# Kernel optimization log

Measured on AMD Instinct MI355X. Metric: run time of the kernel, lower is better.

Reference implementation:

```python
import jax, jax.numpy as jnp
import numpy as np

EMBED_DIM = 1024
HEAD = 16
DK = EMBED_DIM // HEAD  # 64
B, S = 2, 2048
NEG = -1.0e9


def setup_inputs() -> dict:
    key = jax.random.key(0)
    ks = jax.random.split(key, 8)
    d = {
        'query': jax.random.normal(ks[0], (B, S, EMBED_DIM), jnp.float32),
        'key': jax.random.normal(ks[1], (B, S, EMBED_DIM), jnp.float32),
        'value': jax.random.normal(ks[2], (B, S, EMBED_DIM), jnp.float32),
        'masked': jax.random.randint(ks[3], (B, S, S), 0, 2).astype(bool),
        'Wq': jax.random.normal(ks[4], (EMBED_DIM, EMBED_DIM), jnp.float32) / np.sqrt(EMBED_DIM),
        'Wk': jax.random.normal(ks[5], (EMBED_DIM, EMBED_DIM), jnp.float32) / np.sqrt(EMBED_DIM),
        'Wv': jax.random.normal(ks[6], (EMBED_DIM, EMBED_DIM), jnp.float32) / np.sqrt(EMBED_DIM),
        'Wo': jax.random.normal(ks[7], (EMBED_DIM, EMBED_DIM), jnp.float32) / np.sqrt(EMBED_DIM),
    }
    return d


def reference(query, key, value, masked, Wq, Wk, Wv, Wo):
    # projections (bias-free Linear: x @ W), split into heads: [B, H, S, DK]
    def split_heads(x):
        b, s, _ = x.shape
        return x.reshape(b, s, HEAD, DK).transpose(0, 2, 1, 3)

    q = split_heads(query @ Wq)
    k = split_heads(key @ Wk)
    v = split_heads(value @ Wv)

    scale = 1.0 / jnp.sqrt(jnp.asarray(DK, q.dtype))
    scores = jnp.einsum('bhqd,bhkd->bhqk', q, k) * scale
    scores = jnp.where(masked[:, None, :, :], NEG, scores)
    attn = jax.nn.softmax(scores, axis=-1)
    out = jnp.einsum('bhqk,bhkd->bhqd', attn, v)  # [B, H, S, DK]
    out = out.transpose(0, 2, 1, 3).reshape(query.shape[0], -1, EMBED_DIM)
    return out @ Wo
```

## Files before the change

kernel.cpp:

```cpp
#include <hip/hip_runtime.h>
#include <hip/hip_bf16.h>

typedef float f32x4 __attribute__((ext_vector_type(4)));
typedef __bf16 bf16x8 __attribute__((ext_vector_type(8)));

__device__ __forceinline__ unsigned short f2bf(float f){
  unsigned int u = __builtin_bit_cast(unsigned int, f);
  u += 0x7fffu + ((u >> 16) & 1u);
  return (unsigned short)(u >> 16);
}
__device__ __forceinline__ float bf2f(unsigned short h){
  return __builtin_bit_cast(float, (unsigned int)h << 16);
}

__device__ __forceinline__ void glds16(const void* g, void* l){
  __builtin_amdgcn_global_load_lds((const __attribute__((address_space(1))) void*)g,
                                   (__attribute__((address_space(3))) void*)l, 16, 0, 0);
}

__device__ __forceinline__ f32x4 mfma16(bf16x8 a, bf16x8 b, f32x4 c){
  return __builtin_amdgcn_mfma_f32_16x16x32_bf16(a, b, c, 0, 0, 0);
}

#if __has_builtin(__builtin_amdgcn_exp2f)
__device__ __forceinline__ float exp2v(float x){ return __builtin_amdgcn_exp2f(x); }
#else
__device__ __forceinline__ float exp2v(float x){ return exp2f(x); }
#endif

__device__ __forceinline__ unsigned int cvtpk(float a, float b){
  unsigned int r;
  asm("v_cvt_pk_bf16_f32 %0, %1, %2" : "=v"(r) : "v"(a), "v"(b));
  return r;
}

__global__ void detect_kernel(const unsigned int* __restrict__ m, int* __restrict__ flag){
  int t = threadIdx.x;
  int bad = 0;
  for(int i = t; i < 4096; i += 256) bad |= (m[i] > 1u);
  unsigned long long b = __ballot(bad != 0);
  __shared__ int sbuf[4];
  if((t & 63) == 0) sbuf[t >> 6] = (b != 0ull);
  __syncthreads();
  if(t == 0) flag[0] = (sbuf[0] | sbuf[1] | sbuf[2] | sbuf[3]) ? 0 : 1;
}

__global__ void pack_mask_kernel(const unsigned char* __restrict__ m8,
                                 unsigned int* __restrict__ mp,
                                 const int* __restrict__ flag){
  const int wid = threadIdx.x >> 6, lane = threadIdx.x & 63;
  const int row = blockIdx.x * 4 + wid;
  const int is32 = flag[0];
  const int* m32 = (const int*)m8;
  for(int c0 = 0; c0 < 2048; c0 += 64){
    int mv = is32 ? m32[(size_t)row*2048 + c0 + lane]
                  : (int)m8[(size_t)row*2048 + c0 + lane];
    unsigned long long b = __ballot(mv != 0);
    if(lane == 0){
      mp[(size_t)row*64 + (c0 >> 5)]     = (unsigned int)b;
      mp[(size_t)row*64 + (c0 >> 5) + 1] = (unsigned int)(b >> 32);
    }
  }
}

__global__ void cvt_kernel(const float* __restrict__ src, unsigned short* __restrict__ dst){
  int i = blockIdx.x * 256 + threadIdx.x;
  const float4* s = (const float4*)src;
  float4 a = s[2*i], b = s[2*i+1];
  union { unsigned short h[8]; uint4 v; } o;
  o.h[0]=f2bf(a.x); o.h[1]=f2bf(a.y); o.h[2]=f2bf(a.z); o.h[3]=f2bf(a.w);
  o.h[4]=f2bf(b.x); o.h[5]=f2bf(b.y); o.h[6]=f2bf(b.z); o.h[7]=f2bf(b.w);
  ((uint4*)dst)[i] = o.v;
}

__global__ void transW_kernel(const float* __restrict__ Wq, const float* __restrict__ Wk,
                              const float* __restrict__ Wv, const float* __restrict__ Wo,
                              unsigned short* __restrict__ WT){
  const float* W = (blockIdx.y==0)?Wq:(blockIdx.y==1)?Wk:(blockIdx.y==2)?Wv:Wo;
  unsigned short* D = WT + (size_t)blockIdx.y * 1048576;
  int r0 = (blockIdx.x >> 4) * 64, c0 = (blockIdx.x & 15) * 64;
  __shared__ unsigned short T[64][65];
  int t = threadIdx.x;
  {
    int r = t >> 2, cb = (t & 3) * 16;
    const float4* src = (const float4*)(W + (size_t)(r0 + r) * 1024 + (c0 + cb));
    float4 v0 = src[0], v1 = src[1], v2 = src[2], v3 = src[3];
    float vals[16] = {v0.x,v0.y,v0.z,v0.w, v1.x,v1.y,v1.z,v1.w,
                      v2.x,v2.y,v2.z,v2.w, v3.x,v3.y,v3.z,v3.w};
    #pragma unroll
    for(int j=0;j<16;j++) T[cb + j][r] = f2bf(vals[j]);
  }
  __syncthreads();
  {
    int c = t >> 2, rb = (t & 3) * 16;
    union { unsigned short h[16]; uint4 v[2]; } o;
    #pragma unroll
    for(int j=0;j<16;j++) o.h[j] = T[c][rb + j];
    uint4* dp = (uint4*)(D + (size_t)(c0 + c) * 1024 + (r0 + rb));
    dp[0] = o.v[0]; dp[1] = o.v[1];
  }
}

__global__ void transV_kernel(const unsigned short* __restrict__ Vb,
                              unsigned short* __restrict__ Vt){
  const int bh = blockIdx.y, b = bh >> 4, h = bh & 15;
  const int s0 = blockIdx.x * 64;
  __shared__ unsigned short T[64][68];
  const int t = threadIdx.x;
  {
    int r = t >> 2, cb = (t & 3) * 16;
    const uint4* src = (const uint4*)(Vb + (size_t)(b*2048 + s0 + r)*1024 + h*64 + cb);
    union { unsigned short h[16]; uint4 v[2]; } o;
    o.v[0] = src[0]; o.v[1] = src[1];
    uint2* dst = (uint2*)&T[r][cb];
    const uint2* sv = (const uint2*)o.h;
    dst[0]=sv[0]; dst[1]=sv[1]; dst[2]=sv[2]; dst[3]=sv[3];
  }
  __syncthreads();
  {
    int c = t >> 2, sb = (t & 3) * 16;
    union { unsigned short h[16]; uint4 v[2]; } o;
    #pragma unroll
    for(int j=0;j<16;j++) o.h[j] = T[sb + j][c];
    uint4* dp = (uint4*)(Vt + (size_t)(bh*64 + c)*2048 + s0 + sb);
    dp[0] = o.v[0]; dp[1] = o.v[1];
  }
}

template<int OUTF32>
__global__ __launch_bounds__(256,2) void gemm_bt(
    const unsigned short* __restrict__ A0, const unsigned short* __restrict__ A1, const unsigned short* __restrict__ A2,
    const unsigned short* __restrict__ B0, const unsigned short* __restrict__ B1, const unsigned short* __restrict__ B2,
    unsigned short* __restrict__ C0, unsigned short* __restrict__ C1, unsigned short* __restrict__ C2,
    float* __restrict__ Cf)
{
  const unsigned short* A  = (blockIdx.z==0)?A0:(blockIdx.z==1)?A1:A2;
  const unsigned short* BT = (blockIdx.z==0)?B0:(blockIdx.z==1)?B1:B2;
  unsigned short* C        = (blockIdx.z==0)?C0:(blockIdx.z==1)?C1:C2;
  __shared__ unsigned short Asm[128*32];
  __shared__ unsigned short Bsm[128*32];
  const int wid = threadIdx.x >> 6, lane = threadIdx.x & 63;
  const int m0 = blockIdx.x * 128, n0 = blockIdx.y * 128;
  const int wrow = wid >> 1, wcol = wid & 1;
  f32x4 acc[4][4] = {};
  const int sr = lane >> 2;
  const int sc = lane & 3;

  for(int kt = 0; kt < 32; ++kt){
    const int kofs = kt * 32;
    #pragma unroll
    for(int i=0;i<2;i++){
      int r = wid*32 + i*16 + sr;
      int blk = sc ^ (r & 3);
      glds16(A  + (size_t)(m0 + r)*1024 + kofs + blk*8, &Asm[(wid*32 + i*16)*32]);
      glds16(BT + (size_t)(n0 + r)*1024 + kofs + blk*8, &Bsm[(wid*32 + i*16)*32]);
    }
    __syncthreads();
    bf16x8 af[4], bfv[4];
    #pragma unroll
    for(int fm=0; fm<4; fm++){
      int row = wrow*64 + fm*16 + (lane & 15);
      int blk = (lane >> 4) ^ (row & 3);
      af[fm] = *(const bf16x8*)&Asm[row*32 + blk*8];
    }
    #pragma unroll
    for(int fn=0; fn<4; fn++){
      int row = wcol*64 + fn*16 + (lane & 15);
      int blk = (lane >> 4) ^ (row & 3);
      bfv[fn] = *(const bf16x8*)&Bsm[row*32 + blk*8];
    }
    __builtin_amdgcn_s_setprio(1);
    #pragma unroll
    for(int fm=0; fm<4; fm++)
      #pragma unroll
      for(int fn=0; fn<4; fn++)
        acc[fm][fn] = mfma16(af[fm], bfv[fn], acc[fm][fn]);
    __builtin_amdgcn_s_setprio(0);
    __syncthreads();
  }
  #pragma unroll
  for(int fm=0; fm<4; fm++){
    #pragma unroll
    for(int fn=0; fn<4; fn++){
      int col  = n0 + wcol*64 + fn*16 + (lane & 15);
      int rowb = m0 + wrow*64 + fm*16 + (lane >> 4)*4;
      #pragma unroll
      for(int r=0;r<4;r++){
        if(OUTF32) Cf[(size_t)(rowb + r)*1024 + col] = acc[fm][fn][r];
        else       C [(size_t)(rowb + r)*1024 + col] = f2bf(acc[fm][fn][r]);
      }
    }
  }
}

__global__ __launch_bounds__(256,4) void attn_kernel(
    const unsigned short* __restrict__ Q, const unsigned short* __restrict__ K,
    const unsigned short* __restrict__ Vt, unsigned short* __restrict__ O,
    const unsigned int* __restrict__ mp)
{
  __shared__ unsigned short Ksm[2][64*64];
  __shared__ unsigned short Vsm[2][64*64];
  __shared__ unsigned short Psm[4][16][64];
  const int wid = threadIdx.x >> 6, lane = threadIdx.x & 63;
  const int orig = blockIdx.x;
  const int wg = (orig & 7) * 128 + (orig >> 3);
  const int qt = wg & 31, bh = wg >> 5;
  const int b = bh >> 4, h = bh & 15;
  const int q0 = qt * 64;
  const int li = lane & 15, lg = lane >> 4;

  bf16x8 qf[2];
  {
    const unsigned short* qp = Q + (size_t)(b*2048 + q0 + wid*16 + li)*1024 + h*64 + lg*8;
    union { unsigned short s[8]; bf16x8 v; } u0, u1;
    u0.v = *(const bf16x8*)qp; u1.v = *(const bf16x8*)(qp + 32);
    #pragma unroll
    for(int j=0;j<8;j++){
      u0.s[j] = f2bf(bf2f(u0.s[j]) * 0.1803368801111601f);
      u1.s[j] = f2bf(bf2f(u1.s[j]) * 0.1803368801111601f);
    }
    qf[0] = u0.v; qf[1] = u1.v;
  }

  f32x4 oacc[4] = {};
  float mrow = -__builtin_inff();
  float lrow = 0.f;

  const int srow = lane >> 3;
  const int sblk = (lane & 7) ^ srow;
  const int mrowg = b*2048 + q0 + wid*16 + li;
  const int li7 = li & 7;

  #pragma unroll
  for(int i=0;i<2;i++){
    int r = wid*16 + i*8 + srow;
    glds16(K  + (size_t)(b*2048 + r)*1024 + h*64 + sblk*8, &Ksm[0][(wid*16 + i*8)*64]);
    glds16(Vt + (size_t)(bh*64 + r)*2048 + sblk*8,         &Vsm[0][(wid*16 + i*8)*64]);
  }
  uint2 mw = *(const uint2*)&mp[(size_t)mrowg*64];
  uint2 mwn;
  __syncthreads();

  int buf = 0;
  for(int t = 0; t < 32; ++t){
    const int kv0 = t * 64;
    if(t < 31){
      #pragma unroll
      for(int i=0;i<2;i++){
        int r = wid*16 + i*8 + srow;
        glds16(K  + (size_t)(b*2048 + kv0 + 64 + r)*1024 + h*64 + sblk*8, &Ksm[buf^1][(wid*16 + i*8)*64]);
        glds16(Vt + (size_t)(bh*64 + r)*2048 + kv0 + 64 + sblk*8,         &Vsm[buf^1][(wid*16 + i*8)*64]);
      }
      mwn = *(const uint2*)&mp[(size_t)mrowg*64 + (size_t)((kv0 + 64) >> 5)];
    }
    float p[4][4];
    __builtin_amdgcn_s_setprio(1);
    #pragma unroll
    for(int f=0; f<4; f++){
      f32x4 s = {0.f,0.f,0.f,0.f};
      #pragma unroll
      for(int kf=0; kf<2; kf++){
        int blk = (kf*4 + lg) ^ li7;
        bf16x8 kfr = *(const bf16x8*)&Ksm[buf][(f*16 + li)*64 + blk*8];
        s = mfma16(kfr, qf[kf], s);
      }
      #pragma unroll
      for(int j=0;j<4;j++) p[f][j] = s[j];
    }
    __builtin_amdgcn_s_setprio(0);
    #pragma unroll
    for(int f=0; f<4; f++){
      unsigned int w = (f < 2) ? mw.x : mw.y;
      #pragma unroll
      for(int j=0;j<4;j++){
        unsigned int bit = (w >> ((f & 1)*16 + lg*4 + j)) & 1u;
        p[f][j] = bit ? -1.0e9f : p[f][j];
      }
    }
    float tmax;
    {
      float m0 = fmaxf(fmaxf(p[0][0],p[0][1]), fmaxf(p[0][2],p[0][3]));
      float m1 = fmaxf(fmaxf(p[1][0],p[1][1]), fmaxf(p[1][2],p[1][3]));
      float m2 = fmaxf(fmaxf(p[2][0],p[2][1]), fmaxf(p[2][2],p[2][3]));
      float m3 = fmaxf(fmaxf(p[3][0],p[3][1]), fmaxf(p[3][2],p[3][3]));
      tmax = fmaxf(fmaxf(m0,m1), fmaxf(m2,m3));
      tmax = fmaxf(tmax, __shfl_xor(tmax, 16));
      tmax = fmaxf(tmax, __shfl_xor(tmax, 32));
    }
    if(__any(tmax > mrow + 8.f)){
      float mn = fmaxf(mrow, tmax);
      float scal = exp2v(mrow - mn);
      mrow = mn;
      lrow *= scal;
      float so0 = __shfl(scal, lg*4 + 0);
      float so1 = __shfl(scal, lg*4 + 1);
      float so2 = __shfl(scal, lg*4 + 2);
      float so3 = __shfl(scal, lg*4 + 3);
      #pragma unroll
      for(int d=0; d<4; d++){
        oacc[d][0] *= so0; oacc[d][1] *= so1; oacc[d][2] *= so2; oacc[d][3] *= so3;
      }
    }
    {
      float rs = 0.f;
      #pragma unroll
      for(int f=0; f<4; f++){
        float e0 = exp2v(p[f][0] - mrow);
        float e1 = exp2v(p[f][1] - mrow);
        float e2 = exp2v(p[f][2] - mrow);
        float e3 = exp2v(p[f][3] - mrow);
        rs += (e0 + e1) + (e2 + e3);
        unsigned int a0 = cvtpk(e0, e1);
        unsigned int a1 = cvtpk(e2, e3);
        int blk = (f*2 + (lg >> 1)) ^ li7;
        uint2 w2; w2.x = a0; w2.y = a1;
        *(uint2*)&Psm[wid][li][blk*8 + (lg & 1)*4] = w2;
      }
      lrow += rs;
    }
    __builtin_amdgcn_s_setprio(1);
    #pragma unroll
    for(int ks=0; ks<2; ks++){
      bf16x8 pa = *(const bf16x8*)&Psm[wid][li][((ks*4 + lg) ^ li7)*8];
      #pragma unroll
      for(int d=0; d<4; d++){
        int blk = (ks*4 + lg) ^ li7;
        bf16x8 vf = *(const bf16x8*)&Vsm[buf][(d*16 + li)*64 + blk*8];
        oacc[d] = mfma16(pa, vf, oacc[d]);
      }
    }
    __builtin_amdgcn_s_setprio(0);
    __syncthreads();
    mw = mwn;
    buf ^= 1;
  }
  float rs = lrow;
  rs += __shfl_xor(rs, 16);
  rs += __shfl_xor(rs, 32);
  float inv = 1.0f / rs;
  float io0 = __shfl(inv, lg*4 + 0);
  float io1 = __shfl(inv, lg*4 + 1);
  float io2 = __shfl(inv, lg*4 + 2);
  float io3 = __shfl(inv, lg*4 + 3);
  #pragma unroll
  for(int d=0; d<4; d++){
    size_t rb = (size_t)(b*2048 + q0 + wid*16 + lg*4);
    O[(rb+0)*1024 + h*64 + 16*d + li] = f2bf(oacc[d][0] * io0);
    O[(rb+1)*1024 + h*64 + 16*d + li] = f2bf(oacc[d][1] * io1);
    O[(rb+2)*1024 + h*64 + 16*d + li] = f2bf(oacc[d][2] * io2);
    O[(rb+3)*1024 + h*64 + 16*d + li] = f2bf(oacc[d][3] * io3);
  }
}

extern "C" void kernel_launch(void* const* d_in, const int* in_sizes, int n_in,
                              void* d_out, int out_size, void* d_ws, size_t ws_size,
                              hipStream_t stream)
{
  const float* q_in = (const float*)d_in[0];
  const float* k_in = (const float*)d_in[1];
  const float* v_in = (const float*)d_in[2];
  const unsigned char* mask = (const unsigned char*)d_in[3];
  const float* Wq = (const float*)d_in[4];
  const float* Wk = (const float*)d_in[5];
  const float* Wv = (const float*)d_in[6];
  const float* Wo = (const float*)d_in[7];

  char* ws = (char*)d_ws;
  const size_t MB = 1024*1024;
  int* flag          = (int*)ws;
  unsigned short* XQ = (unsigned short*)(ws + 256);
  unsigned short* XK = (unsigned short*)(ws + 256 + 8*MB);
  unsigned short* XV = (unsigned short*)(ws + 256 + 16*MB);
  unsigned short* WT = (unsigned short*)(ws + 256 + 24*MB);
  unsigned short* Qb = (unsigned short*)(ws + 256 + 32*MB);
  unsigned short* Kb = (unsigned short*)(ws + 256 + 40*MB);
  unsigned short* Vb = (unsigned short*)(ws + 256 + 48*MB);
  unsigned short* Ob = XQ;
  unsigned short* Vt = XK;
  unsigned int*   mpk= (unsigned int*)XV;

  detect_kernel<<<1, 256, 0, stream>>>((const unsigned int*)mask, flag);
  cvt_kernel<<<2048, 256, 0, stream>>>(q_in, XQ);
  cvt_kernel<<<2048, 256, 0, stream>>>(k_in, XK);
  cvt_kernel<<<2048, 256, 0, stream>>>(v_in, XV);
  transW_kernel<<<dim3(256,4), 256, 0, stream>>>(Wq, Wk, Wv, Wo, WT);
  gemm_bt<0><<<dim3(32,8,3), 256, 0, stream>>>(XQ, XK, XV,
                                               WT, WT + 1048576, WT + 2097152,
                                               Qb, Kb, Vb, nullptr);
  transV_kernel<<<dim3(32,32), 256, 0, stream>>>(Vb, Vt);
  pack_mask_kernel<<<1024, 256, 0, stream>>>(mask, mpk, flag);
  attn_kernel<<<1024, 256, 0, stream>>>(Qb, Kb, Vt, Ob, mpk);
  gemm_bt<1><<<dim3(32,8,1), 256, 0, stream>>>(Ob, Ob, Ob,
                                               WT + 3*1048576, WT + 3*1048576, WT + 3*1048576,
                                               nullptr, nullptr, nullptr, (float*)d_out);
}
```

Before: 171.5 us.

## Widen GEMM K-tile, merge input conversions, and interleave attention P writes with PV MFMAs

The projection GEMM now stages 64-wide K tiles (16 iterations instead of 32) with an 8-way XOR swizzle, which halves the barrier count per output tile at the cost of doubling LDS per block. The three fp32-to-bf16 conversion launches are merged into one 3D-grid launch writing contiguous 8MB slices. In attention, the P staging buffer is halved and each 32-column half of P is written and immediately consumed by its PV MFMAs, reducing LDS footprint and shortening live ranges. The merged conversion relies on XQ/XK/XV being laid out contiguously at 8MB offsets.

```diff
diff --git a/kernel.cpp b/kernel.cpp
--- a/kernel.cpp
+++ b/kernel.cpp
@@ -63,14 +63,17 @@
   }
 }
 
-__global__ void cvt_kernel(const float* __restrict__ src, unsigned short* __restrict__ dst){
+__global__ void cvt3_kernel(const float* __restrict__ qs, const float* __restrict__ ks,
+                            const float* __restrict__ vs, unsigned short* __restrict__ dst){
+  const float* src = (blockIdx.y==0)?qs:(blockIdx.y==1)?ks:vs;
+  unsigned short* d = dst + (size_t)blockIdx.y * 4194304;
   int i = blockIdx.x * 256 + threadIdx.x;
   const float4* s = (const float4*)src;
   float4 a = s[2*i], b = s[2*i+1];
   union { unsigned short h[8]; uint4 v; } o;
   o.h[0]=f2bf(a.x); o.h[1]=f2bf(a.y); o.h[2]=f2bf(a.z); o.h[3]=f2bf(a.w);
   o.h[4]=f2bf(b.x); o.h[5]=f2bf(b.y); o.h[6]=f2bf(b.z); o.h[7]=f2bf(b.w);
-  ((uint4*)dst)[i] = o.v;
+  ((uint4*)d)[i] = o.v;
 }
 
 __global__ void transW_kernel(const float* __restrict__ Wq, const float* __restrict__ Wk,
@@ -137,53 +140,57 @@
   const unsigned short* A  = (blockIdx.z==0)?A0:(blockIdx.z==1)?A1:A2;
   const unsigned short* BT = (blockIdx.z==0)?B0:(blockIdx.z==1)?B1:B2;
   unsigned short* C        = (blockIdx.z==0)?C0:(blockIdx.z==1)?C1:C2;
-  __shared__ unsigned short Asm[128*32];
-  __shared__ unsigned short Bsm[128*32];
+  __shared__ unsigned short Asm[128*64];
+  __shared__ unsigned short Bsm[128*64];
   const int wid = threadIdx.x >> 6, lane = threadIdx.x & 63;
   const int m0 = blockIdx.x * 128, n0 = blockIdx.y * 128;
   const int wrow = wid >> 1, wcol = wid & 1;
+  const int li = lane & 15, lg = lane >> 4, li7 = lane & 7;
   f32x4 acc[4][4] = {};
-  const int sr = lane >> 2;
-  const int sc = lane & 3;
-
-  for(int kt = 0; kt < 32; ++kt){
-    const int kofs = kt * 32;
-    #pragma unroll
-    for(int i=0;i<2;i++){
-      int r = wid*32 + i*16 + sr;
-      int blk = sc ^ (r & 3);
-      glds16(A  + (size_t)(m0 + r)*1024 + kofs + blk*8, &Asm[(wid*32 + i*16)*32]);
-      glds16(BT + (size_t)(n0 + r)*1024 + kofs + blk*8, &Bsm[(wid*32 + i*16)*32]);
+  const int sr = lane >> 3;
+  const int sc = lane & 7;
+
+  for(int kt = 0; kt < 16; ++kt){
+    const int kofs = kt * 64;
+    #pragma unroll
+    for(int i=0;i<4;i++){
+      int r = wid*32 + i*8 + sr;
+      int blk = sc ^ sr;
+      glds16(A  + (size_t)(m0 + r)*1024 + kofs + blk*8, &Asm[(wid*32 + i*8)*64]);
+      glds16(BT + (size_t)(n0 + r)*1024 + kofs + blk*8, &Bsm[(wid*32 + i*8)*64]);
     }
     __syncthreads();
-    bf16x8 af[4], bfv[4];
-    #pragma unroll
-    for(int fm=0; fm<4; fm++){
-      int row = wrow*64 + fm*16 + (lane & 15);
-      int blk = (lane >> 4) ^ (row & 3);
-      af[fm] = *(const bf16x8*)&Asm[row*32 + blk*8];
-    }
-    #pragma unroll
-    for(int fn=0; fn<4; fn++){
-      int row = wcol*64 + fn*16 + (lane & 15);
-      int blk = (lane >> 4) ^ (row & 3);
-      bfv[fn] = *(const bf16x8*)&Bsm[row*32 + blk*8];
-    }
-    __builtin_amdgcn_s_setprio(1);
-    #pragma unroll
-    for(int fm=0; fm<4; fm++)
-      #pragma unroll
-      for(int fn=0; fn<4; fn++)
-        acc[fm][fn] = mfma16(af[fm], bfv[fn], acc[fm][fn]);
-    __builtin_amdgcn_s_setprio(0);
+    #pragma unroll
+    for(int kk=0; kk<2; kk++){
+      bf16x8 af[4], bfv[4];
+      #pragma unroll
+      for(int fm=0; fm<4; fm++){
+        int row = wrow*64 + fm*16 + li;
+        int blk = (kk*4 + lg) ^ li7;
+        af[fm] = *(const bf16x8*)&Asm[row*64 + blk*8];
+      }
+      #pragma unroll
+      for(int fn=0; fn<4; fn++){
+        int row = wcol*64 + fn*16 + li;
+        int blk = (kk*4 + lg) ^ li7;
+        bfv[fn] = *(const bf16x8*)&Bsm[row*64 + blk*8];
+      }
+      __builtin_amdgcn_s_setprio(1);
+      #pragma unroll
+      for(int fm=0; fm<4; fm++)
+        #pragma unroll
+        for(int fn=0; fn<4; fn++)
+          acc[fm][fn] = mfma16(af[fm], bfv[fn], acc[fm][fn]);
+      __builtin_amdgcn_s_setprio(0);
+    }
     __syncthreads();
   }
   #pragma unroll
   for(int fm=0; fm<4; fm++){
     #pragma unroll
     for(int fn=0; fn<4; fn++){
-      int col  = n0 + wcol*64 + fn*16 + (lane & 15);
-      int rowb = m0 + wrow*64 + fm*16 + (lane >> 4)*4;
+      int col  = n0 + wcol*64 + fn*16 + li;
+      int rowb = m0 + wrow*64 + fm*16 + lg*4;
       #pragma unroll
       for(int r=0;r<4;r++){
         if(OUTF32) Cf[(size_t)(rowb + r)*1024 + col] = acc[fm][fn][r];
@@ -200,7 +207,7 @@
 {
   __shared__ unsigned short Ksm[2][64*64];
   __shared__ unsigned short Vsm[2][64*64];
-  __shared__ unsigned short Psm[4][16][64];
+  __shared__ unsigned short Psm[4][16][32];
   const int wid = threadIdx.x >> 6, lane = threadIdx.x & 63;
   const int orig = blockIdx.x;
   const int wg = (orig & 7) * 128 + (orig >> 3);
@@ -208,6 +215,7 @@
   const int b = bh >> 4, h = bh & 15;
   const int q0 = qt * 64;
   const int li = lane & 15, lg = lane >> 4;
+  const int li7 = li & 7, li3 = li & 3;
 
   bf16x8 qf[2];
   {
@@ -229,7 +237,6 @@
   const int srow = lane >> 3;
   const int sblk = (lane & 7) ^ srow;
   const int mrowg = b*2048 + q0 + wid*16 + li;
-  const int li7 = li & 7;
 
   #pragma unroll
   for(int i=0;i<2;i++){
@@ -301,10 +308,12 @@
         oacc[d][0] *= so0; oacc[d][1] *= so1; oacc[d][2] *= so2; oacc[d][3] *= so3;
       }
     }
-    {
-      float rs = 0.f;
-      #pragma unroll
-      for(int f=0; f<4; f++){
+    float rs = 0.f;
+    #pragma unroll
+    for(int ks=0; ks<2; ks++){
+      #pragma unroll
+      for(int fl=0; fl<2; fl++){
+        const int f = ks*2 + fl;
         float e0 = exp2v(p[f][0] - mrow);
         float e1 = exp2v(p[f][1] - mrow);
         float e2 = exp2v(p[f][2] - mrow);
@@ -312,24 +321,21 @@
         rs += (e0 + e1) + (e2 + e3);
         unsigned int a0 = cvtpk(e0, e1);
         unsigned int a1 = cvtpk(e2, e3);
-        int blk = (f*2 + (lg >> 1)) ^ li7;
+        int blk = (fl*2 + (lg >> 1)) ^ li3;
         uint2 w2; w2.x = a0; w2.y = a1;
         *(uint2*)&Psm[wid][li][blk*8 + (lg & 1)*4] = w2;
       }
-      lrow += rs;
-    }
-    __builtin_amdgcn_s_setprio(1);
-    #pragma unroll
-    for(int ks=0; ks<2; ks++){
-      bf16x8 pa = *(const bf16x8*)&Psm[wid][li][((ks*4 + lg) ^ li7)*8];
+      bf16x8 pa = *(const bf16x8*)&Psm[wid][li][(lg ^ li3)*8];
+      __builtin_amdgcn_s_setprio(1);
       #pragma unroll
       for(int d=0; d<4; d++){
         int blk = (ks*4 + lg) ^ li7;
         bf16x8 vf = *(const bf16x8*)&Vsm[buf][(d*16 + li)*64 + blk*8];
         oacc[d] = mfma16(pa, vf, oacc[d]);
       }
-    }
-    __builtin_amdgcn_s_setprio(0);
+      __builtin_amdgcn_s_setprio(0);
+    }
+    lrow += rs;
     __syncthreads();
     mw = mwn;
     buf ^= 1;
@@ -380,9 +386,7 @@
   unsigned int*   mpk= (unsigned int*)XV;
 
   detect_kernel<<<1, 256, 0, stream>>>((const unsigned int*)mask, flag);
-  cvt_kernel<<<2048, 256, 0, stream>>>(q_in, XQ);
-  cvt_kernel<<<2048, 256, 0, stream>>>(k_in, XK);
-  cvt_kernel<<<2048, 256, 0, stream>>>(v_in, XV);
+  cvt3_kernel<<<dim3(2048,3), 256, 0, stream>>>(q_in, k_in, v_in, XQ);
   transW_kernel<<<dim3(256,4), 256, 0, stream>>>(Wq, Wk, Wv, Wo, WT);
   gemm_bt<0><<<dim3(32,8,3), 256, 0, stream>>>(XQ, XK, XV,
                                                WT, WT + 1048576, WT + 2097152,
```

After: 161.7 us. 5.7% less time.
